# Optimization experiments

Hardware: AMD Instinct MI355X
Metric: run time of the kernel (lower is better)

The kernel has to match this reference:

```python
import jax, jax.numpy as jnp
import numpy as np

NUM_HEADS = 16


def setup_inputs() -> dict:
    key = jax.random.key(0)
    k1, k2, k3, k4 = jax.random.split(key, 4)
    B, N, D = 4, 2048, 1024
    inputs = jax.random.normal(k1, (B, N, D), dtype=jnp.float32)
    w_in = jax.random.normal(k2, (3 * D, D), dtype=jnp.float32) * (D ** -0.5)
    w_out = jax.random.normal(k3, (D, D), dtype=jnp.float32) * (D ** -0.5)
    b_out = jax.random.normal(k4, (D,), dtype=jnp.float32) * 0.02
    return {"inputs": inputs, "w_in": w_in, "w_out": w_out, "b_out": b_out}


def reference(inputs, w_in, w_out, b_out):
    B, N, D = inputs.shape
    H = NUM_HEADS
    Hd = D // H
    # in_proj (torch Linear: x @ W.T), split into Q,K,V
    qkv = jnp.einsum('bnd,ed->bne', inputs, w_in)  # [B,N,3D]
    q, k, v = jnp.split(qkv, 3, axis=-1)
    # [B,H,N,Hd]
    q = q.reshape(B, N, H, Hd).transpose(0, 2, 1, 3)
    k = k.reshape(B, N, H, Hd).transpose(0, 2, 1, 3)
    v = v.reshape(B, N, H, Hd).transpose(0, 2, 1, 3)
    scores = jnp.einsum('bhqd,bhkd->bhqk', q, k) * (Hd ** -0.5)
    causal = jnp.triu(jnp.ones((N, N), dtype=bool), k=1)  # True above diagonal
    scores = jnp.where(causal, -jnp.inf, scores)
    attn = jax.nn.softmax(scores, axis=-1)
    out = jnp.einsum('bhqk,bhkd->bhqd', attn, v)  # [B,H,N,Hd]
    out = out.transpose(0, 2, 1, 3).reshape(B, N, D)
    return jnp.einsum('bnd,ed->bne', out, w_out) + b_out
```

## Files before the change

kernel.cpp:

```cpp
#include <hip/hip_runtime.h>
#include <hip/hip_bf16.h>
#include <cstdint>

typedef __hip_bfloat16 bf16;
typedef short short8 __attribute__((ext_vector_type(8)));
typedef float f32x4 __attribute__((ext_vector_type(4)));

#define AS1C(p) ((const __attribute__((address_space(1))) void*)(p))
#define AS3(p)  ((__attribute__((address_space(3))) void*)(p))

__device__ __forceinline__ float b2f(short s) {
    union { unsigned u; float f; } c; c.u = ((unsigned)(unsigned short)s) << 16; return c.f;
}

template<int CTRL>
__device__ __forceinline__ float dppf(float x) {
    return __int_as_float(__builtin_amdgcn_update_dpp(
        0, __float_as_int(x), CTRL, 0xF, 0xF, true));
}
__device__ __forceinline__ float row_sum16(float x) {
    x += dppf<0xB1>(x);
    x += dppf<0x4E>(x);
    x += dppf<0x141>(x);
    x += dppf<0x140>(x);
    return x;
}

__global__ void cvt_f32_bf16(const float* __restrict__ src, bf16* __restrict__ dst, int n4)
{
    int i = blockIdx.x * blockDim.x + threadIdx.x;
    if (i >= n4) return;
    float4 v = ((const float4*)src)[i];
    __align__(8) bf16 t[4] = { __float2bfloat16(v.x), __float2bfloat16(v.y),
                               __float2bfloat16(v.z), __float2bfloat16(v.w) };
    ((uint2*)dst)[i] = *(const uint2*)t;
}

template<bool SPLIT_V, bool HAS_BIAS, typename OUT_T>
__global__ __launch_bounds__(256, 2)
void gemm_bt(const bf16* __restrict__ A, int lda, const bf16* __restrict__ B,
             const float* __restrict__ bias, OUT_T* __restrict__ C, int ldc,
             bf16* __restrict__ vt, int M, int N, int K)
{
    __shared__ __align__(16) bf16 As[128 * 32];
    __shared__ __align__(16) bf16 Bs[128 * 32];
    const int tid  = threadIdx.x;
    const int wave = tid >> 6, lane = tid & 63;
    const int wm = wave >> 1, wn = wave & 1;
    const int quad = lane >> 4, l15 = lane & 15;
    const int tile_m = blockIdx.y, tile_n = blockIdx.x;

    const bf16* Ap = A + (size_t)tile_m * 128 * lda;
    const bf16* Bp = B + (size_t)tile_n * 128 * K;

    const int srow = lane >> 2;
    const int scol = (lane & 3) * 8;

    f32x4 acc[4][4];
    #pragma unroll
    for (int i = 0; i < 4; i++)
        #pragma unroll
        for (int j = 0; j < 4; j++) acc[i][j] = (f32x4){0.f, 0.f, 0.f, 0.f};

    for (int k0 = 0; k0 < K; k0 += 32) {
        #pragma unroll
        for (int cc = 0; cc < 2; cc++) {
            int c = wave + cc * 4;
            const bf16* ga = Ap + (size_t)(c * 16 + srow) * lda + k0 + scol;
            __builtin_amdgcn_global_load_lds(AS1C(ga), AS3(&As[c * 16 * 32]), 16, 0, 0);
            const bf16* gb = Bp + (size_t)(c * 16 + srow) * K + k0 + scol;
            __builtin_amdgcn_global_load_lds(AS1C(gb), AS3(&Bs[c * 16 * 32]), 16, 0, 0);
        }
        __syncthreads();

        short8 af[4], bfr[4];
        #pragma unroll
        for (int mi = 0; mi < 4; mi++)
            af[mi] = *(const short8*)&As[(wm * 64 + mi * 16 + l15) * 32 + quad * 8];
        #pragma unroll
        for (int ni = 0; ni < 4; ni++)
            bfr[ni] = *(const short8*)&Bs[(wn * 64 + ni * 16 + l15) * 32 + quad * 8];
        #pragma unroll
        for (int mi = 0; mi < 4; mi++)
            #pragma unroll
            for (int ni = 0; ni < 4; ni++)
                acc[mi][ni] = __builtin_amdgcn_mfma_f32_16x16x32_bf16(
                    af[mi], bfr[ni], acc[mi][ni], 0, 0, 0);
        __syncthreads();
    }

    const bool vtile = SPLIT_V && (tile_n * 128 >= 2048);
    #pragma unroll
    for (int mi = 0; mi < 4; mi++) {
        #pragma unroll
        for (int ni = 0; ni < 4; ni++) {
            int coln = tile_n * 128 + wn * 64 + ni * 16 + l15;
            if (!vtile) {
                float bv = HAS_BIAS ? bias[coln] : 0.f;
                #pragma unroll
                for (int r = 0; r < 4; r++) {
                    int row = tile_m * 128 + wm * 64 + mi * 16 + quad * 4 + r;
                    float v = acc[mi][ni][r] + bv;
                    if constexpr (__is_same(OUT_T, float))
                        C[(size_t)row * ldc + coln] = v;
                    else
                        C[(size_t)row * ldc + coln] = __float2bfloat16(v);
                }
            } else {
                int vcol = coln - 2048;
                int row0 = tile_m * 128 + wm * 64 + mi * 16 + quad * 4;
                int bb = row0 >> 11, n0 = row0 & 2047;
                __align__(8) bf16 t4[4];
                #pragma unroll
                for (int r = 0; r < 4; r++) t4[r] = __float2bfloat16(acc[mi][ni][r]);
                *(uint2*)&vt[((size_t)(bb * 1024 + vcol)) * 2048 + n0] = *(const uint2*)t4;
            }
        }
    }
}

__global__ __launch_bounds__(256, 3)
void flash_attn(bf16* __restrict__ qkv, const bf16* __restrict__ vt)
{
    const int idx = blockIdx.x;
    const int qt  = 15 - (idx >> 6);
    const int bh  = idx & 63;
    const int b   = bh >> 4, h = bh & 15;
    const int tid = threadIdx.x;
    const int wave = tid >> 6, lane = tid & 63;
    const int quad = lane >> 4, l15 = lane & 15;

    __shared__ __align__(16) bf16 Ks[2][64 * 64];
    __shared__ __align__(16) bf16 Vs[2][64 * 64];
    __shared__ __align__(16) bf16 Ps[4][2][16][72];

    const int q0   = qt * 128;
    const int rowA = wave * 32;
    const size_t rs = 2048;

    short8 qa[2][2];
    #pragma unroll
    for (int mi = 0; mi < 2; mi++)
        #pragma unroll
        for (int kw = 0; kw < 2; kw++) {
            const bf16* qr = qkv + (size_t)(b * 2048 + q0 + rowA + mi * 16 + l15) * rs
                           + h * 64 + kw * 32 + quad * 8;
            short8 t = *(const short8*)qr;
            #pragma unroll
            for (int e = 0; e < 8; e++)
                t[e] = (short)__bfloat16_as_ushort(__float2bfloat16(b2f(t[e]) * 0.125f));
            qa[mi][kw] = t;
        }

    f32x4 o[2][4];
    #pragma unroll
    for (int mi = 0; mi < 2; mi++)
        #pragma unroll
        for (int nt = 0; nt < 4; nt++) o[mi][nt] = (f32x4){0.f, 0.f, 0.f, 0.f};
    float lsum[2][4] = {{0.f,0.f,0.f,0.f},{0.f,0.f,0.f,0.f}};

    const bf16* kbase = qkv + (size_t)(b * 2048) * rs + 1024 + h * 64;
    const bf16* vbase = vt + (size_t)(bh * 64) * 2048;

    const int srow8  = lane >> 3;
    const int schunk = (lane & 7) ^ srow8;

    #define STAGE(J, BUF)                                                          \
        {   const int jj = (J);                                                    \
            _Pragma("unroll")                                                      \
            for (int i = 0; i < 2; i++) {                                          \
                int rr_ = wave * 16 + i * 8 + srow8;                               \
                const bf16* gk = kbase + (size_t)(jj * 64 + rr_) * rs + schunk * 8;\
                __builtin_amdgcn_global_load_lds(AS1C(gk),                         \
                    AS3(&Ks[BUF][(wave * 16 + i * 8) * 64]), 16, 0, 0);            \
                const bf16* gv = vbase + (size_t)rr_ * 2048 + jj * 64 + schunk * 8;\
                __builtin_amdgcn_global_load_lds(AS1C(gv),                         \
                    AS3(&Vs[BUF][(wave * 16 + i * 8) * 64]), 16, 0, 0);            \
            }                                                                      \
        }

    STAGE(0, 0)
    const int jmax = 2 * qt + 1;
    for (int j = 0; j <= jmax; j++) {
        __syncthreads();
        const int buf = j & 1;
        if (j < jmax) STAGE(j + 1, buf ^ 1)

        if (j * 64 > q0 + rowA + 31) continue;

        f32x4 s[2][4];
        #pragma unroll
        for (int mi = 0; mi < 2; mi++)
            #pragma unroll
            for (int tc = 0; tc < 4; tc++) s[mi][tc] = (f32x4){0.f,0.f,0.f,0.f};
        #pragma unroll
        for (int kw = 0; kw < 2; kw++) {
            short8 kb[4];
            #pragma unroll
            for (int tc = 0; tc < 4; tc++)
                kb[tc] = *(const short8*)&Ks[buf][(tc * 16 + l15) * 64 +
                         (((kw * 4 + quad) ^ (l15 & 7)) * 8)];
            #pragma unroll
            for (int mi = 0; mi < 2; mi++)
                #pragma unroll
                for (int tc = 0; tc < 4; tc++)
                    s[mi][tc] = __builtin_amdgcn_mfma_f32_16x16x32_bf16(
                        qa[mi][kw], kb[tc], s[mi][tc], 0, 0, 0);
        }
        if (j * 64 + 63 > q0 + rowA) {
            #pragma unroll
            for (int mi = 0; mi < 2; mi++)
                #pragma unroll
                for (int tc = 0; tc < 4; tc++)
                    #pragma unroll
                    for (int rr = 0; rr < 4; rr++)
                        if (j * 64 + tc * 16 + l15 >
                            q0 + rowA + mi * 16 + quad * 4 + rr)
                            s[mi][tc][rr] = -INFINITY;
        }
        #pragma unroll
        for (int mi = 0; mi < 2; mi++) {
            #pragma unroll
            for (int tc = 0; tc < 4; tc++)
                #pragma unroll
                for (int rr = 0; rr < 4; rr++)
                    s[mi][tc][rr] = __expf(s[mi][tc][rr]);
            #pragma unroll
            for (int rr = 0; rr < 4; rr++)
                lsum[mi][rr] += (s[mi][0][rr] + s[mi][1][rr]) +
                                (s[mi][2][rr] + s[mi][3][rr]);
        }
        #pragma unroll
        for (int mi = 0; mi < 2; mi++)
            #pragma unroll
            for (int tc = 0; tc < 4; tc++)
                #pragma unroll
                for (int rr = 0; rr < 4; rr++)
                    Ps[wave][mi][quad * 4 + rr][tc * 16 + l15] =
                        __float2bfloat16(s[mi][tc][rr]);
        #pragma unroll
        for (int kw = 0; kw < 2; kw++) {
            short8 vb[4];
            #pragma unroll
            for (int nt = 0; nt < 4; nt++)
                vb[nt] = *(const short8*)&Vs[buf][(nt * 16 + l15) * 64 +
                         (((kw * 4 + quad) ^ (l15 & 7)) * 8)];
            short8 pa[2];
            #pragma unroll
            for (int mi = 0; mi < 2; mi++)
                pa[mi] = *(const short8*)&Ps[wave][mi][l15][kw * 32 + quad * 8];
            #pragma unroll
            for (int mi = 0; mi < 2; mi++)
                #pragma unroll
                for (int nt = 0; nt < 4; nt++)
                    o[mi][nt] = __builtin_amdgcn_mfma_f32_16x16x32_bf16(
                        pa[mi], vb[nt], o[mi][nt], 0, 0, 0);
        }
    }

    #pragma unroll
    for (int mi = 0; mi < 2; mi++)
        #pragma unroll
        for (int rr = 0; rr < 4; rr++) {
            float inv = 1.f / row_sum16(lsum[mi][rr]);
            int row = b * 2048 + q0 + rowA + mi * 16 + quad * 4 + rr;
            #pragma unroll
            for (int nt = 0; nt < 4; nt++) {
                int col = h * 64 + nt * 16 + l15;
                qkv[(size_t)row * rs + col] = __float2bfloat16(o[mi][nt][rr] * inv);
            }
        }
}

extern "C" void kernel_launch(void* const* d_in, const int* in_sizes, int n_in,
                              void* d_out, int out_size, void* d_ws, size_t ws_size,
                              hipStream_t stream)
{
    const float* x     = (const float*)d_in[0];
    const float* w_in  = (const float*)d_in[1];
    const float* w_out = (const float*)d_in[2];
    const float* b_out = (const float*)d_in[3];
    float* out = (float*)d_out;

    bf16* qkv = (bf16*)d_ws;
    bf16* vt  = qkv + (size_t)8192 * 2048;
    bf16* xb  = vt  + (size_t)4096 * 2048;
    bf16* wib = xb  + (size_t)8192 * 1024;
    bf16* wob = wib + (size_t)3072 * 1024;

    cvt_f32_bf16<<<(8192 * 1024 / 4 + 255) / 256, 256, 0, stream>>>(x, xb, 8192 * 1024 / 4);
    cvt_f32_bf16<<<(3072 * 1024 / 4 + 255) / 256, 256, 0, stream>>>(w_in, wib, 3072 * 1024 / 4);
    cvt_f32_bf16<<<(1024 * 1024 / 4 + 255) / 256, 256, 0, stream>>>(w_out, wob, 1024 * 1024 / 4);

    gemm_bt<true, false, bf16><<<dim3(3072 / 128, 8192 / 128), 256, 0, stream>>>(
        xb, 1024, wib, nullptr, qkv, 2048, vt, 8192, 3072, 1024);
    flash_attn<<<1024, 256, 0, stream>>>(qkv, vt);
    gemm_bt<false, true, float><<<dim3(1024 / 128, 8192 / 128), 256, 0, stream>>>(
        qkv, 2048, wob, b_out, out, 1024, nullptr, 8192, 1024, 1024);
}
```

Measured before the change: 253.1 us.

## Double-buffer GEMM LDS tiles and swap grid axes for M-major block order

The GEMM kernel now keeps two LDS stages for A and B. It issues the global-to-LDS load for the next K slice before computing the current one, and drops the trailing barrier so each iteration has one sync. The grid is also transposed so consecutive blocks walk along M and share the same weight tile, which may change L2 reuse. This doubles LDS use per block and could affect occupancy. There is also a possible hazard: the prefetch into the other buffer is not waited on before the next barrier, since global_load_lds needs vmcnt waits.

```diff
diff --git a/kernel.cpp b/kernel.cpp
--- a/kernel.cpp
+++ b/kernel.cpp
@@ -42,13 +42,13 @@
              const float* __restrict__ bias, OUT_T* __restrict__ C, int ldc,
              bf16* __restrict__ vt, int M, int N, int K)
 {
-    __shared__ __align__(16) bf16 As[128 * 32];
-    __shared__ __align__(16) bf16 Bs[128 * 32];
+    __shared__ __align__(16) bf16 As[2][128 * 32];
+    __shared__ __align__(16) bf16 Bs[2][128 * 32];
     const int tid  = threadIdx.x;
     const int wave = tid >> 6, lane = tid & 63;
     const int wm = wave >> 1, wn = wave & 1;
     const int quad = lane >> 4, l15 = lane & 15;
-    const int tile_m = blockIdx.y, tile_n = blockIdx.x;
+    const int tile_m = blockIdx.x, tile_n = blockIdx.y;
 
     const bf16* Ap = A + (size_t)tile_m * 128 * lda;
     const bf16* Bp = B + (size_t)tile_n * 128 * K;
@@ -62,32 +62,42 @@
         #pragma unroll
         for (int j = 0; j < 4; j++) acc[i][j] = (f32x4){0.f, 0.f, 0.f, 0.f};
 
-    for (int k0 = 0; k0 < K; k0 += 32) {
-        #pragma unroll
-        for (int cc = 0; cc < 2; cc++) {
-            int c = wave + cc * 4;
-            const bf16* ga = Ap + (size_t)(c * 16 + srow) * lda + k0 + scol;
-            __builtin_amdgcn_global_load_lds(AS1C(ga), AS3(&As[c * 16 * 32]), 16, 0, 0);
-            const bf16* gb = Bp + (size_t)(c * 16 + srow) * K + k0 + scol;
-            __builtin_amdgcn_global_load_lds(AS1C(gb), AS3(&Bs[c * 16 * 32]), 16, 0, 0);
-        }
+    #define GSTAGE(KI, BUF)                                                        \
+        {   const int k0_ = (KI) * 32;                                             \
+            _Pragma("unroll")                                                      \
+            for (int cc = 0; cc < 2; cc++) {                                       \
+                int c = wave + cc * 4;                                             \
+                const bf16* ga = Ap + (size_t)(c * 16 + srow) * lda + k0_ + scol;  \
+                __builtin_amdgcn_global_load_lds(AS1C(ga),                         \
+                    AS3(&As[BUF][c * 16 * 32]), 16, 0, 0);                         \
+                const bf16* gb = Bp + (size_t)(c * 16 + srow) * K + k0_ + scol;    \
+                __builtin_amdgcn_global_load_lds(AS1C(gb),                         \
+                    AS3(&Bs[BUF][c * 16 * 32]), 16, 0, 0);                         \
+            }                                                                      \
+        }
+
+    const int nk = K >> 5;
+    GSTAGE(0, 0)
+    for (int ki = 0; ki < nk; ki++) {
         __syncthreads();
+        const int buf = ki & 1;
+        if (ki + 1 < nk) GSTAGE(ki + 1, buf ^ 1)
 
         short8 af[4], bfr[4];
         #pragma unroll
         for (int mi = 0; mi < 4; mi++)
-            af[mi] = *(const short8*)&As[(wm * 64 + mi * 16 + l15) * 32 + quad * 8];
+            af[mi] = *(const short8*)&As[buf][(wm * 64 + mi * 16 + l15) * 32 + quad * 8];
         #pragma unroll
         for (int ni = 0; ni < 4; ni++)
-            bfr[ni] = *(const short8*)&Bs[(wn * 64 + ni * 16 + l15) * 32 + quad * 8];
+            bfr[ni] = *(const short8*)&Bs[buf][(wn * 64 + ni * 16 + l15) * 32 + quad * 8];
         #pragma unroll
         for (int mi = 0; mi < 4; mi++)
             #pragma unroll
             for (int ni = 0; ni < 4; ni++)
                 acc[mi][ni] = __builtin_amdgcn_mfma_f32_16x16x32_bf16(
                     af[mi], bfr[ni], acc[mi][ni], 0, 0, 0);
-        __syncthreads();
     }
+    #undef GSTAGE
 
     const bool vtile = SPLIT_V && (tile_n * 128 >= 2048);
     #pragma unroll
@@ -257,6 +267,7 @@
                         pa[mi], vb[nt], o[mi][nt], 0, 0, 0);
         }
     }
+    #undef STAGE
 
     #pragma unroll
     for (int mi = 0; mi < 2; mi++)
@@ -292,9 +303,9 @@
     cvt_f32_bf16<<<(3072 * 1024 / 4 + 255) / 256, 256, 0, stream>>>(w_in, wib, 3072 * 1024 / 4);
     cvt_f32_bf16<<<(1024 * 1024 / 4 + 255) / 256, 256, 0, stream>>>(w_out, wob, 1024 * 1024 / 4);
 
-    gemm_bt<true, false, bf16><<<dim3(3072 / 128, 8192 / 128), 256, 0, stream>>>(
+    gemm_bt<true, false, bf16><<<dim3(8192 / 128, 3072 / 128), 256, 0, stream>>>(
         xb, 1024, wib, nullptr, qkv, 2048, vt, 8192, 3072, 1024);
     flash_attn<<<1024, 256, 0, stream>>>(qkv, vt);
-    gemm_bt<false, true, float><<<dim3(1024 / 128, 8192 / 128), 256, 0, stream>>>(
+    gemm_bt<false, true, float><<<dim3(8192 / 128, 1024 / 128), 256, 0, stream>>>(
         qkv, 2048, wob, b_out, out, 1024, nullptr, 8192, 1024, 1024);
 }
```

After: 245.8 us. 1.03x faster.
